# Performance work log

Measured on AMD Instinct MI355X. Metric: run time of the kernel, lower is better.

## Reference

```python
import jax, jax.numpy as jnp
import numpy as np

N, E = 100000, 1600000
IN, HID, OUT = 128, 64, 64
BN_EPS = 1e-5


def setup_inputs() -> dict:
    key = jax.random.key(0)
    ks = jax.random.split(key, 6)
    x = jax.random.normal(ks[0], (N, IN), dtype=jnp.float32)
    edge_index = jax.random.randint(ks[1], (2, E), 0, N, dtype=jnp.int32)
    W1 = jax.random.normal(ks[2], (IN, HID), dtype=jnp.float32) / np.sqrt(IN).astype(np.float32)
    b1 = jnp.zeros((HID,), jnp.float32)
    bn_weight = jnp.ones((HID,), jnp.float32)
    bn_bias = jnp.zeros((HID,), jnp.float32)
    W2 = jax.random.normal(ks[3], (HID, OUT), dtype=jnp.float32) / np.sqrt(HID).astype(np.float32)
    b2 = jnp.zeros((OUT,), jnp.float32)
    return {"x": x, "edge_index": edge_index, "W1": W1, "b1": b1,
            "bn_weight": bn_weight, "bn_bias": bn_bias, "W2": W2, "b2": b2}


def _gcn_conv(x, W, b, src, dst, deg_inv_sqrt):
    # PyG GCNConv: linear first, then symmetric-normalized aggregation with self-loops.
    h = x @ W                                        # [N, out]
    norm = deg_inv_sqrt[src] * deg_inv_sqrt[dst]     # [E]
    agg = jax.ops.segment_sum(h[src] * norm[:, None], dst, num_segments=h.shape[0])
    # self-loop contribution: norm = 1/deg
    agg = agg + h * (deg_inv_sqrt * deg_inv_sqrt)[:, None]
    return agg + b


def reference(x, edge_index, W1, b1, bn_weight, bn_bias, W2, b2):
    src, dst = edge_index[0], edge_index[1]
    # degree including self-loop (GCNConv add_self_loops=True, edge_weight=1)
    deg = jax.ops.segment_sum(jnp.ones((E,), x.dtype), dst, num_segments=N) + 1.0
    deg_inv_sqrt = jax.lax.rsqrt(deg)
    h = _gcn_conv(x, W1, b1, src, dst, deg_inv_sqrt)
    # BatchNorm1d (training-mode batch statistics, biased variance)
    mean = jnp.mean(h, axis=0)
    var = jnp.var(h, axis=0)
    h = (h - mean) * jax.lax.rsqrt(var + BN_EPS) * bn_weight + bn_bias
    h = jax.nn.relu(h)
    # dropout: inference mode (identity)
    return _gcn_conv(h, W2, b2, src, dst, deg_inv_sqrt)
```

## Files before the change

### kernel.cpp

```cpp
#include <hip/hip_runtime.h>

#define N_NODES 100000
#define E_EDGES 1600000
#define IN_F    128
#define HID_F   64
#define OUT_F   64
#define BN_EPS  1e-5f
#define NBUK    391
#define CHUNK   6250
#define NGBLK   3125

__device__ __forceinline__ float bflo(unsigned int u) { return __uint_as_float(u << 16); }
__device__ __forceinline__ float bfhi(unsigned int u) { return __uint_as_float(u & 0xFFFF0000u); }
__device__ __forceinline__ unsigned int pack2bf(float a, float b) {
    unsigned int ua = __float_as_uint(a), ub = __float_as_uint(b);
    ua = (ua + 0x7fffu + ((ua >> 16) & 1u)) >> 16;
    ub = (ub + 0x7fffu + ((ub >> 16) & 1u)) >> 16;
    return ua | (ub << 16);
}
#define ADD8(A, u)                                           \
    do {                                                     \
        A[0] += bflo((u).x); A[1] += bfhi((u).x);            \
        A[2] += bflo((u).y); A[3] += bfhi((u).y);            \
        A[4] += bflo((u).z); A[5] += bfhi((u).z);            \
        A[6] += bflo((u).w); A[7] += bfhi((u).w);            \
    } while (0)

__global__ __launch_bounds__(512) void k_chist(const int* __restrict__ dstv,
                                               int* __restrict__ chist) {
    __shared__ int h[NBUK];
    const int tid = threadIdx.x;
    const int e0 = blockIdx.x * CHUNK;
    for (int b = tid; b < NBUK; b += 512) h[b] = 0;
    __syncthreads();
    for (int t = tid; t < CHUNK; t += 512)
        atomicAdd(&h[dstv[e0 + t] >> 8], 1);
    __syncthreads();
    for (int b = tid; b < NBUK; b += 512)
        if (h[b]) atomicAdd(&chist[b], h[b]);
}

__global__ __launch_bounds__(512) void k_cscan(int* __restrict__ coff,
                                               int* __restrict__ ccur) {
    __shared__ int sh[512];
    const int tid = threadIdx.x;
    int v = (tid < NBUK) ? coff[tid] : 0;
    sh[tid] = v;
    __syncthreads();
    for (int off = 1; off < 512; off <<= 1) {
        int t = (tid >= off) ? sh[tid - off] : 0;
        __syncthreads();
        sh[tid] += t;
        __syncthreads();
    }
    int excl = sh[tid] - v;
    if (tid < NBUK) { coff[tid] = excl; ccur[tid] = excl; }
    if (tid == 0) coff[NBUK] = E_EDGES;
}

__global__ __launch_bounds__(512) void k_bucket(const int* __restrict__ srcv,
                                                const int* __restrict__ dstv,
                                                int* __restrict__ ccur,
                                                unsigned int* __restrict__ aux) {
    __shared__ int dl[CHUNK];
    __shared__ int hist[NBUK], base[NBUK], lcur[NBUK];
    const int tid = threadIdx.x;
    const int e0 = blockIdx.x * CHUNK;
    for (int b = tid; b < NBUK; b += 512) hist[b] = 0;
    __syncthreads();
    for (int t = tid; t < CHUNK; t += 512) {
        int d = dstv[e0 + t];
        dl[t] = d;
        atomicAdd(&hist[d >> 8], 1);
    }
    __syncthreads();
    for (int b = tid; b < NBUK; b += 512) {
        int h = hist[b];
        if (h) base[b] = atomicAdd(&ccur[b], h);
        lcur[b] = 0;
    }
    __syncthreads();
    for (int t = tid; t < CHUNK; t += 512) {
        int d = dl[t];
        int b = d >> 8;
        int off = atomicAdd(&lcur[b], 1);
        aux[base[b] + off] = ((unsigned int)srcv[e0 + t] << 8) | (unsigned int)(d & 255);
    }
}

__global__ __launch_bounds__(256) void k_csrnode(const int* __restrict__ coff,
                                                 const unsigned int* __restrict__ aux,
                                                 int* __restrict__ rowptr,
                                                 float* __restrict__ dis,
                                                 int* __restrict__ csr_src) {
    __shared__ int c0[256], sc[256], cur[256];
    const int tid = threadIdx.x;
    const int n0 = blockIdx.x * 256;
    const int nn = min(256, N_NODES - n0);
    const int estart = coff[blockIdx.x];
    const int eend   = coff[blockIdx.x + 1];
    c0[tid] = 0;
    __syncthreads();
    for (int e = estart + tid; e < eend; e += 256)
        atomicAdd(&c0[aux[e] & 255], 1);
    __syncthreads();
    int v = c0[tid];
    sc[tid] = v;
    __syncthreads();
    for (int off = 1; off < 256; off <<= 1) {
        int t = (tid >= off) ? sc[tid - off] : 0;
        __syncthreads();
        sc[tid] += t;
        __syncthreads();
    }
    int excl = sc[tid] - v;
    if (tid < nn) {
        int p = estart + excl;
        rowptr[n0 + tid] = p;
        cur[tid] = p;
        dis[n0 + tid] = rsqrtf((float)v + 1.0f);
    }
    if (blockIdx.x == NBUK - 1 && tid == 0) rowptr[N_NODES] = E_EDGES;
    __syncthreads();
    for (int e = estart + tid; e < eend; e += 256) {
        unsigned int u = aux[e];
        int pos = atomicAdd(&cur[u & 255], 1);
        csr_src[pos] = (int)(u >> 8);
    }
}

__global__ __launch_bounds__(256) void k_gemm1(const float* __restrict__ x,
                                               const float* __restrict__ W1,
                                               const float* __restrict__ dis,
                                               unsigned short* __restrict__ hs1) {
    __shared__ float Ws[IN_F][HID_F];
    __shared__ float As[64][68];
    const int tid = threadIdx.x;
    const int r0 = blockIdx.x * 64;

#pragma unroll
    for (int p = 0; p < 8; ++p) {
        int idx = p * 256 + tid;
        ((float4*)&Ws[0][0])[idx] = ((const float4*)W1)[idx];
    }

    const int tx = tid & 15, ty = tid >> 4;
    float acc[4][4] = {};

    for (int kk = 0; kk < IN_F; kk += 64) {
        __syncthreads();
#pragma unroll
        for (int p = 0; p < 4; ++p) {
            int idx = p * 256 + tid;
            int row = idx >> 4;
            int c4  = idx & 15;
            float4 v = make_float4(0.f, 0.f, 0.f, 0.f);
            if (r0 + row < N_NODES)
                v = ((const float4*)(x + (size_t)(r0 + row) * IN_F + kk))[c4];
            *(float4*)&As[row][c4 * 4] = v;
        }
        __syncthreads();
#pragma unroll 4
        for (int k2 = 0; k2 < 64; ++k2) {
            int k = kk + k2;
            float4 b = *(const float4*)&Ws[k][tx * 4];
            float a0 = As[ty * 4 + 0][k2];
            float a1 = As[ty * 4 + 1][k2];
            float a2 = As[ty * 4 + 2][k2];
            float a3 = As[ty * 4 + 3][k2];
            acc[0][0] = fmaf(a0, b.x, acc[0][0]); acc[0][1] = fmaf(a0, b.y, acc[0][1]);
            acc[0][2] = fmaf(a0, b.z, acc[0][2]); acc[0][3] = fmaf(a0, b.w, acc[0][3]);
            acc[1][0] = fmaf(a1, b.x, acc[1][0]); acc[1][1] = fmaf(a1, b.y, acc[1][1]);
            acc[1][2] = fmaf(a1, b.z, acc[1][2]); acc[1][3] = fmaf(a1, b.w, acc[1][3]);
            acc[2][0] = fmaf(a2, b.x, acc[2][0]); acc[2][1] = fmaf(a2, b.y, acc[2][1]);
            acc[2][2] = fmaf(a2, b.z, acc[2][2]); acc[2][3] = fmaf(a2, b.w, acc[2][3]);
            acc[3][0] = fmaf(a3, b.x, acc[3][0]); acc[3][1] = fmaf(a3, b.y, acc[3][1]);
            acc[3][2] = fmaf(a3, b.z, acc[3][2]); acc[3][3] = fmaf(a3, b.w, acc[3][3]);
        }
    }
#pragma unroll
    for (int j = 0; j < 4; ++j) {
        int row = r0 + ty * 4 + j;
        if (row < N_NODES) {
            float d = dis[row];
            uint2 o;
            o.x = pack2bf(acc[j][0] * d, acc[j][1] * d);
            o.y = pack2bf(acc[j][2] * d, acc[j][3] * d);
            *(uint2*)&hs1[(size_t)row * HID_F + tx * 4] = o;
        }
    }
}

__global__ __launch_bounds__(256) void k_gather1(const int* __restrict__ rowptr,
                                                 const int* __restrict__ csr_src,
                                                 const unsigned short* __restrict__ hsb,
                                                 const float* __restrict__ dis,
                                                 const float* __restrict__ b1,
                                                 float* __restrict__ agg,
                                                 float* __restrict__ partials) {
    const int tid = threadIdx.x;
    const int g = tid >> 3, q = tid & 7;
    const int n = blockIdx.x * 32 + g;
    const uint4* __restrict__ hs16 = (const uint4*)hsb;

    const int start = rowptr[n], end = rowptr[n + 1];
    float A0[8] = {}, A1[8] = {}, A2[8] = {}, A3[8] = {};
    {
        uint4 u = hs16[(size_t)n * 8 + q];
        ADD8(A0, u);
    }
    int i = start;
    for (; i + 3 < end; i += 4) {
        int s0 = csr_src[i + 0], s1 = csr_src[i + 1];
        int s2 = csr_src[i + 2], s3 = csr_src[i + 3];
        uint4 u0 = hs16[(size_t)s0 * 8 + q];
        uint4 u1 = hs16[(size_t)s1 * 8 + q];
        uint4 u2 = hs16[(size_t)s2 * 8 + q];
        uint4 u3 = hs16[(size_t)s3 * 8 + q];
        ADD8(A0, u0); ADD8(A1, u1); ADD8(A2, u2); ADD8(A3, u3);
    }
    for (; i < end; ++i) {
        uint4 u = hs16[(size_t)csr_src[i] * 8 + q];
        ADD8(A0, u);
    }
    const float d = dis[n];
    const float4 blo = ((const float4*)b1)[q * 2];
    const float4 bhi = ((const float4*)b1)[q * 2 + 1];
    float o[8];
    o[0] = fmaf(d, A0[0] + A1[0] + A2[0] + A3[0], blo.x);
    o[1] = fmaf(d, A0[1] + A1[1] + A2[1] + A3[1], blo.y);
    o[2] = fmaf(d, A0[2] + A1[2] + A2[2] + A3[2], blo.z);
    o[3] = fmaf(d, A0[3] + A1[3] + A2[3] + A3[3], blo.w);
    o[4] = fmaf(d, A0[4] + A1[4] + A2[4] + A3[4], bhi.x);
    o[5] = fmaf(d, A0[5] + A1[5] + A2[5] + A3[5], bhi.y);
    o[6] = fmaf(d, A0[6] + A1[6] + A2[6] + A3[6], bhi.z);
    o[7] = fmaf(d, A0[7] + A1[7] + A2[7] + A3[7], bhi.w);
    float4* ag = (float4*)(agg + (size_t)n * HID_F + q * 8);
    ag[0] = make_float4(o[0], o[1], o[2], o[3]);
    ag[1] = make_float4(o[4], o[5], o[6], o[7]);

    __shared__ float4 redA[256], redB[256];
    redA[tid] = make_float4(o[0], o[1], o[2], o[3]);
    redB[tid] = make_float4(o[4], o[5], o[6], o[7]);
    __syncthreads();
    for (int s = 128; s >= 8; s >>= 1) {
        if (tid < s) {
            redA[tid].x += redA[tid + s].x; redA[tid].y += redA[tid + s].y;
            redA[tid].z += redA[tid + s].z; redA[tid].w += redA[tid + s].w;
            redB[tid].x += redB[tid + s].x; redB[tid].y += redB[tid + s].y;
            redB[tid].z += redB[tid + s].z; redB[tid].w += redB[tid + s].w;
        }
        __syncthreads();
    }
    float4* pr = (float4*)(partials + (size_t)blockIdx.x * 128);
    if (tid < 8) { pr[tid * 2] = redA[tid]; pr[tid * 2 + 1] = redB[tid]; }
    __syncthreads();
    redA[tid] = make_float4(o[0] * o[0], o[1] * o[1], o[2] * o[2], o[3] * o[3]);
    redB[tid] = make_float4(o[4] * o[4], o[5] * o[5], o[6] * o[6], o[7] * o[7]);
    __syncthreads();
    for (int s = 128; s >= 8; s >>= 1) {
        if (tid < s) {
            redA[tid].x += redA[tid + s].x; redA[tid].y += redA[tid + s].y;
            redA[tid].z += redA[tid + s].z; redA[tid].w += redA[tid + s].w;
            redB[tid].x += redB[tid + s].x; redB[tid].y += redB[tid + s].y;
            redB[tid].z += redB[tid + s].z; redB[tid].w += redB[tid + s].w;
        }
        __syncthreads();
    }
    if (tid < 8) { pr[16 + tid * 2] = redA[tid]; pr[16 + tid * 2 + 1] = redB[tid]; }
}

__global__ __launch_bounds__(256) void k_bnfinal(const float* __restrict__ partials,
                                                 float* __restrict__ bnstats) {
    const int tid = threadIdx.x;
    const int col = tid & 127;
    const int half = tid >> 7;
    float s = 0.f;
    for (int r = blockIdx.x * 2 + half; r < NGBLK; r += 128)
        s += partials[(size_t)r * 128 + col];
    __shared__ float sh[256];
    sh[tid] = s;
    __syncthreads();
    if (tid < 128) unsafeAtomicAdd(&bnstats[col], sh[tid] + sh[tid + 128]);
}

__global__ __launch_bounds__(256) void k_gemm2(const float* __restrict__ agg1,
                                               const float* __restrict__ W2,
                                               const float* __restrict__ dis,
                                               const float* __restrict__ bnw,
                                               const float* __restrict__ bnb,
                                               const float* __restrict__ bnstats,
                                               unsigned short* __restrict__ hs2) {
    __shared__ float Ws[HID_F][OUT_F];
    __shared__ float As[64][68];
    __shared__ float scale_s[64], shift_s[64];
    const int tid = threadIdx.x;
    const int r0 = blockIdx.x * 64;

    if (tid < 64) {
        const float invN = 1.0f / (float)N_NODES;
        float mean = bnstats[tid] * invN;
        float var  = bnstats[64 + tid] * invN - mean * mean;
        float sc   = bnw[tid] * rsqrtf(var + BN_EPS);
        scale_s[tid] = sc;
        shift_s[tid] = fmaf(-mean, sc, bnb[tid]);
    }
#pragma unroll
    for (int p = 0; p < 4; ++p) {
        int idx = p * 256 + tid;
        ((float4*)&Ws[0][0])[idx] = ((const float4*)W2)[idx];
    }
    __syncthreads();
#pragma unroll
    for (int p = 0; p < 4; ++p) {
        int idx = p * 256 + tid;
        int row = idx >> 4;
        int c4  = idx & 15;
        float4 v = make_float4(0.f, 0.f, 0.f, 0.f);
        if (r0 + row < N_NODES) {
            v = ((const float4*)(agg1 + (size_t)(r0 + row) * HID_F))[c4];
            int k0 = c4 * 4;
            v.x = fmaxf(fmaf(v.x, scale_s[k0 + 0], shift_s[k0 + 0]), 0.f);
            v.y = fmaxf(fmaf(v.y, scale_s[k0 + 1], shift_s[k0 + 1]), 0.f);
            v.z = fmaxf(fmaf(v.z, scale_s[k0 + 2], shift_s[k0 + 2]), 0.f);
            v.w = fmaxf(fmaf(v.w, scale_s[k0 + 3], shift_s[k0 + 3]), 0.f);
        }
        *(float4*)&As[row][c4 * 4] = v;
    }
    __syncthreads();
    const int tx = tid & 15, ty = tid >> 4;
    float acc[4][4] = {};
#pragma unroll 4
    for (int k = 0; k < HID_F; ++k) {
        float4 b = *(const float4*)&Ws[k][tx * 4];
        float a0 = As[ty * 4 + 0][k];
        float a1 = As[ty * 4 + 1][k];
        float a2 = As[ty * 4 + 2][k];
        float a3 = As[ty * 4 + 3][k];
        acc[0][0] = fmaf(a0, b.x, acc[0][0]); acc[0][1] = fmaf(a0, b.y, acc[0][1]);
        acc[0][2] = fmaf(a0, b.z, acc[0][2]); acc[0][3] = fmaf(a0, b.w, acc[0][3]);
        acc[1][0] = fmaf(a1, b.x, acc[1][0]); acc[1][1] = fmaf(a1, b.y, acc[1][1]);
        acc[1][2] = fmaf(a1, b.z, acc[1][2]); acc[1][3] = fmaf(a1, b.w, acc[1][3]);
        acc[2][0] = fmaf(a2, b.x, acc[2][0]); acc[2][1] = fmaf(a2, b.y, acc[2][1]);
        acc[2][2] = fmaf(a2, b.z, acc[2][2]); acc[2][3] = fmaf(a2, b.w, acc[2][3]);
        acc[3][0] = fmaf(a3, b.x, acc[3][0]); acc[3][1] = fmaf(a3, b.y, acc[3][1]);
        acc[3][2] = fmaf(a3, b.z, acc[3][2]); acc[3][3] = fmaf(a3, b.w, acc[3][3]);
    }
#pragma unroll
    for (int j = 0; j < 4; ++j) {
        int row = r0 + ty * 4 + j;
        if (row < N_NODES) {
            float d = dis[row];
            uint2 o;
            o.x = pack2bf(acc[j][0] * d, acc[j][1] * d);
            o.y = pack2bf(acc[j][2] * d, acc[j][3] * d);
            *(uint2*)&hs2[(size_t)row * OUT_F + tx * 4] = o;
        }
    }
}

__global__ __launch_bounds__(256) void k_gather2(const int* __restrict__ rowptr,
                                                 const int* __restrict__ csr_src,
                                                 const unsigned short* __restrict__ hsb,
                                                 const float* __restrict__ dis,
                                                 const float* __restrict__ b2,
                                                 float* __restrict__ out) {
    const int tid = threadIdx.x;
    const int g = tid >> 3, q = tid & 7;
    const int n = blockIdx.x * 32 + g;
    const uint4* __restrict__ hs16 = (const uint4*)hsb;

    const int start = rowptr[n], end = rowptr[n + 1];
    float A0[8] = {}, A1[8] = {}, A2[8] = {}, A3[8] = {};
    {
        uint4 u = hs16[(size_t)n * 8 + q];
        ADD8(A0, u);
    }
    int i = start;
    for (; i + 3 < end; i += 4) {
        int s0 = csr_src[i + 0], s1 = csr_src[i + 1];
        int s2 = csr_src[i + 2], s3 = csr_src[i + 3];
        uint4 u0 = hs16[(size_t)s0 * 8 + q];
        uint4 u1 = hs16[(size_t)s1 * 8 + q];
        uint4 u2 = hs16[(size_t)s2 * 8 + q];
        uint4 u3 = hs16[(size_t)s3 * 8 + q];
        ADD8(A0, u0); ADD8(A1, u1); ADD8(A2, u2); ADD8(A3, u3);
    }
    for (; i < end; ++i) {
        uint4 u = hs16[(size_t)csr_src[i] * 8 + q];
        ADD8(A0, u);
    }
    const float d = dis[n];
    const float4 blo = ((const float4*)b2)[q * 2];
    const float4 bhi = ((const float4*)b2)[q * 2 + 1];
    float4 o0, o1;
    o0.x = fmaf(d, A0[0] + A1[0] + A2[0] + A3[0], blo.x);
    o0.y = fmaf(d, A0[1] + A1[1] + A2[1] + A3[1], blo.y);
    o0.z = fmaf(d, A0[2] + A1[2] + A2[2] + A3[2], blo.z);
    o0.w = fmaf(d, A0[3] + A1[3] + A2[3] + A3[3], blo.w);
    o1.x = fmaf(d, A0[4] + A1[4] + A2[4] + A3[4], bhi.x);
    o1.y = fmaf(d, A0[5] + A1[5] + A2[5] + A3[5], bhi.y);
    o1.z = fmaf(d, A0[6] + A1[6] + A2[6] + A3[6], bhi.z);
    o1.w = fmaf(d, A0[7] + A1[7] + A2[7] + A3[7], bhi.w);
    float4* op = (float4*)(out + (size_t)n * OUT_F + q * 8);
    op[0] = o0;
    op[1] = o1;
}

extern "C" void kernel_launch(void* const* d_in, const int* in_sizes, int n_in,
                              void* d_out, int out_size, void* d_ws, size_t ws_size,
                              hipStream_t stream) {
    const float* x   = (const float*)d_in[0];
    const int*   ei  = (const int*)d_in[1];
    const float* W1  = (const float*)d_in[2];
    const float* b1  = (const float*)d_in[3];
    const float* bnw = (const float*)d_in[4];
    const float* bnb = (const float*)d_in[5];
    const float* W2  = (const float*)d_in[6];
    const float* b2  = (const float*)d_in[7];
    float* out = (float*)d_out;

    float* ws = (float*)d_ws;
    float*        dis     = ws;
    int*          rowptr  = (int*)(ws + 100352);
    int*          coff    = (int*)(ws + 100352 + 100608);
    int*          ccur    = (int*)(ws + 100352 + 100608 + 512);
    float*        bnstats = ws + 100352 + 100608 + 512 + 512;
    int*          csr_src = (int*)(ws + 100352 + 100608 + 512 + 512 + 128);
    float*        bufA    = ws + 100352 + 100608 + 512 + 512 + 128 + 1600000;
    float*        bufB    = bufA + (size_t)N_NODES * HID_F;
    unsigned int*  aux  = (unsigned int*)bufA;
    unsigned short* hsb = (unsigned short*)bufA;
    float* partials = out;

    const int* srcv = ei;
    const int* dstv = ei + E_EDGES;

    hipMemsetAsync(coff, 0, (NBUK + 1) * sizeof(int), stream);
    hipMemsetAsync(bnstats, 0, 128 * sizeof(float), stream);

    k_chist  <<<256, 512, 0, stream>>>(dstv, coff);
    k_cscan  <<<1, 512, 0, stream>>>(coff, ccur);
    k_bucket <<<256, 512, 0, stream>>>(srcv, dstv, ccur, aux);
    k_csrnode<<<NBUK, 256, 0, stream>>>(coff, aux, rowptr, dis, csr_src);

    k_gemm1  <<<(N_NODES + 63) / 64, 256, 0, stream>>>(x, W1, dis, hsb);
    k_gather1<<<NGBLK, 256, 0, stream>>>(rowptr, csr_src, hsb, dis, b1, bufB, partials);
    k_bnfinal<<<64, 256, 0, stream>>>(partials, bnstats);
    k_gemm2  <<<(N_NODES + 63) / 64, 256, 0, stream>>>(bufB, W2, dis, bnw, bnb, bnstats, hsb);
    k_gather2<<<NGBLK, 256, 0, stream>>>(rowptr, csr_src, hsb, dis, b2, out);
}
```

Measured before the change: 275.7 us.

## Use bf16 MFMA for both node-feature GEMMs with LDS-staged coalesced output

Replaces the scalar FP32 FMA tiles in both dense GEMM kernels with bf16 MFMA 16x16x32 instructions. Inputs and weights are converted to bf16 in shared memory, and results are staged through LDS so global stores are 16-byte coalesced. The intent is to cut compute and LDS traffic in the GEMM stages. In exchange, the GEMM inputs lose precision to bf16, and each block transposes the weights with scalar stores.

```diff
diff --git a/kernel.cpp b/kernel.cpp
--- a/kernel.cpp
+++ b/kernel.cpp
@@ -9,6 +9,10 @@
 #define NBUK    391
 #define CHUNK   6250
 #define NGBLK   3125
+#define NMBLK   1563
+
+typedef __bf16 bf16x8 __attribute__((ext_vector_type(8)));
+typedef float  f32x4  __attribute__((ext_vector_type(4)));
 
 __device__ __forceinline__ float bflo(unsigned int u) { return __uint_as_float(u << 16); }
 __device__ __forceinline__ float bfhi(unsigned int u) { return __uint_as_float(u & 0xFFFF0000u); }
@@ -18,6 +22,10 @@
     ub = (ub + 0x7fffu + ((ub >> 16) & 1u)) >> 16;
     return ua | (ub << 16);
 }
+__device__ __forceinline__ unsigned short bf1(float a) {
+    unsigned int ua = __float_as_uint(a);
+    return (unsigned short)((ua + 0x7fffu + ((ua >> 16) & 1u)) >> 16);
+}
 #define ADD8(A, u)                                           \
     do {                                                     \
         A[0] += bflo((u).x); A[1] += bfhi((u).x);            \
@@ -133,61 +141,64 @@
                                                const float* __restrict__ W1,
                                                const float* __restrict__ dis,
                                                unsigned short* __restrict__ hs1) {
-    __shared__ float Ws[IN_F][HID_F];
-    __shared__ float As[64][68];
+    __shared__ unsigned short Asb[64 * 136];
+    __shared__ unsigned short Btb[64 * 136];
+    __shared__ unsigned short Cc[64 * 72];
+    __shared__ float disS[64];
     const int tid = threadIdx.x;
     const int r0 = blockIdx.x * 64;
 
-#pragma unroll
-    for (int p = 0; p < 8; ++p) {
+    if (tid < 64) disS[tid] = (r0 + tid < N_NODES) ? dis[r0 + tid] : 0.f;
+
+    const float4* x4 = (const float4*)x;
+#pragma unroll
+    for (int p = 0; p < 4; ++p) {
+        int idx8 = p * 256 + tid;
+        int row = idx8 >> 4, c8 = idx8 & 15;
+        float4 v0 = make_float4(0.f, 0.f, 0.f, 0.f), v1 = v0;
+        if (r0 + row < N_NODES) {
+            v0 = x4[(size_t)(r0 + row) * 32 + c8 * 2];
+            v1 = x4[(size_t)(r0 + row) * 32 + c8 * 2 + 1];
+        }
+        uint4 u;
+        u.x = pack2bf(v0.x, v0.y); u.y = pack2bf(v0.z, v0.w);
+        u.z = pack2bf(v1.x, v1.y); u.w = pack2bf(v1.z, v1.w);
+        *(uint4*)&Asb[row * 136 + c8 * 8] = u;
+    }
+    for (int idx = tid; idx < IN_F * HID_F; idx += 256) {
+        int k = idx >> 6, n = idx & 63;
+        Btb[n * 136 + k] = bf1(W1[idx]);
+    }
+    __syncthreads();
+
+    const int wv = tid >> 6, lane = tid & 63;
+    const int m = lane & 15, quad = lane >> 4;
+    const int arow = wv * 16 + m;
+    f32x4 acc[4] = {};
+#pragma unroll
+    for (int ks = 0; ks < 4; ++ks) {
+        int k0 = ks * 32 + quad * 8;
+        bf16x8 af = *(const bf16x8*)&Asb[arow * 136 + k0];
+#pragma unroll
+        for (int c = 0; c < 4; ++c) {
+            bf16x8 bfr = *(const bf16x8*)&Btb[(c * 16 + m) * 136 + k0];
+            acc[c] = __builtin_amdgcn_mfma_f32_16x16x32_bf16(af, bfr, acc[c], 0, 0, 0);
+        }
+    }
+#pragma unroll
+    for (int c = 0; c < 4; ++c)
+#pragma unroll
+        for (int r = 0; r < 4; ++r) {
+            int rl = wv * 16 + quad * 4 + r;
+            Cc[rl * 72 + c * 16 + m] = bf1(acc[c][r] * disS[rl]);
+        }
+    __syncthreads();
+#pragma unroll
+    for (int p = 0; p < 2; ++p) {
         int idx = p * 256 + tid;
-        ((float4*)&Ws[0][0])[idx] = ((const float4*)W1)[idx];
-    }
-
-    const int tx = tid & 15, ty = tid >> 4;
-    float acc[4][4] = {};
-
-    for (int kk = 0; kk < IN_F; kk += 64) {
-        __syncthreads();
-#pragma unroll
-        for (int p = 0; p < 4; ++p) {
-            int idx = p * 256 + tid;
-            int row = idx >> 4;
-            int c4  = idx & 15;
-            float4 v = make_float4(0.f, 0.f, 0.f, 0.f);
-            if (r0 + row < N_NODES)
-                v = ((const float4*)(x + (size_t)(r0 + row) * IN_F + kk))[c4];
-            *(float4*)&As[row][c4 * 4] = v;
-        }
-        __syncthreads();
-#pragma unroll 4
-        for (int k2 = 0; k2 < 64; ++k2) {
-            int k = kk + k2;
-            float4 b = *(const float4*)&Ws[k][tx * 4];
-            float a0 = As[ty * 4 + 0][k2];
-            float a1 = As[ty * 4 + 1][k2];
-            float a2 = As[ty * 4 + 2][k2];
-            float a3 = As[ty * 4 + 3][k2];
-            acc[0][0] = fmaf(a0, b.x, acc[0][0]); acc[0][1] = fmaf(a0, b.y, acc[0][1]);
-            acc[0][2] = fmaf(a0, b.z, acc[0][2]); acc[0][3] = fmaf(a0, b.w, acc[0][3]);
-            acc[1][0] = fmaf(a1, b.x, acc[1][0]); acc[1][1] = fmaf(a1, b.y, acc[1][1]);
-            acc[1][2] = fmaf(a1, b.z, acc[1][2]); acc[1][3] = fmaf(a1, b.w, acc[1][3]);
-            acc[2][0] = fmaf(a2, b.x, acc[2][0]); acc[2][1] = fmaf(a2, b.y, acc[2][1]);
-            acc[2][2] = fmaf(a2, b.z, acc[2][2]); acc[2][3] = fmaf(a2, b.w, acc[2][3]);
-            acc[3][0] = fmaf(a3, b.x, acc[3][0]); acc[3][1] = fmaf(a3, b.y, acc[3][1]);
-            acc[3][2] = fmaf(a3, b.z, acc[3][2]); acc[3][3] = fmaf(a3, b.w, acc[3][3]);
-        }
-    }
-#pragma unroll
-    for (int j = 0; j < 4; ++j) {
-        int row = r0 + ty * 4 + j;
-        if (row < N_NODES) {
-            float d = dis[row];
-            uint2 o;
-            o.x = pack2bf(acc[j][0] * d, acc[j][1] * d);
-            o.y = pack2bf(acc[j][2] * d, acc[j][3] * d);
-            *(uint2*)&hs1[(size_t)row * HID_F + tx * 4] = o;
-        }
+        int row = idx >> 3, c8 = idx & 7;
+        if (r0 + row < N_NODES)
+            *(uint4*)&hs1[(size_t)(r0 + row) * 64 + c8 * 8] = *(uint4*)&Cc[row * 72 + c8 * 8];
     }
 }
 
@@ -291,9 +302,10 @@
                                                const float* __restrict__ bnb,
                                                const float* __restrict__ bnstats,
                                                unsigned short* __restrict__ hs2) {
-    __shared__ float Ws[HID_F][OUT_F];
-    __shared__ float As[64][68];
-    __shared__ float scale_s[64], shift_s[64];
+    __shared__ unsigned short Ab[64 * 72];
+    __shared__ unsigned short Bt2[64 * 72];
+    __shared__ unsigned short Cc[64 * 72];
+    __shared__ float scale_s[64], shift_s[64], disS[64];
     const int tid = threadIdx.x;
     const int r0 = blockIdx.x * 64;
 
@@ -304,58 +316,60 @@
         float sc   = bnw[tid] * rsqrtf(var + BN_EPS);
         scale_s[tid] = sc;
         shift_s[tid] = fmaf(-mean, sc, bnb[tid]);
-    }
+        disS[tid] = (r0 + tid < N_NODES) ? dis[r0 + tid] : 0.f;
+    }
+    for (int idx = tid; idx < HID_F * OUT_F; idx += 256) {
+        int k = idx >> 6, n = idx & 63;
+        Bt2[n * 72 + k] = bf1(W2[idx]);
+    }
+    __syncthreads();
+
+    const float4* a4 = (const float4*)agg1;
 #pragma unroll
     for (int p = 0; p < 4; ++p) {
+        int idx4 = p * 256 + tid;
+        int row = idx4 >> 4, c4 = idx4 & 15;
+        float4 v = make_float4(0.f, 0.f, 0.f, 0.f);
+        if (r0 + row < N_NODES) v = a4[(size_t)(r0 + row) * 16 + c4];
+        int k0 = c4 * 4;
+        v.x = fmaxf(fmaf(v.x, scale_s[k0 + 0], shift_s[k0 + 0]), 0.f);
+        v.y = fmaxf(fmaf(v.y, scale_s[k0 + 1], shift_s[k0 + 1]), 0.f);
+        v.z = fmaxf(fmaf(v.z, scale_s[k0 + 2], shift_s[k0 + 2]), 0.f);
+        v.w = fmaxf(fmaf(v.w, scale_s[k0 + 3], shift_s[k0 + 3]), 0.f);
+        uint2 u;
+        u.x = pack2bf(v.x, v.y); u.y = pack2bf(v.z, v.w);
+        *(uint2*)&Ab[row * 72 + c4 * 4] = u;
+    }
+    __syncthreads();
+
+    const int wv = tid >> 6, lane = tid & 63;
+    const int m = lane & 15, quad = lane >> 4;
+    const int arow = wv * 16 + m;
+    f32x4 acc[4] = {};
+#pragma unroll
+    for (int ks = 0; ks < 2; ++ks) {
+        int k0 = ks * 32 + quad * 8;
+        bf16x8 af = *(const bf16x8*)&Ab[arow * 72 + k0];
+#pragma unroll
+        for (int c = 0; c < 4; ++c) {
+            bf16x8 bfr = *(const bf16x8*)&Bt2[(c * 16 + m) * 72 + k0];
+            acc[c] = __builtin_amdgcn_mfma_f32_16x16x32_bf16(af, bfr, acc[c], 0, 0, 0);
+        }
+    }
+#pragma unroll
+    for (int c = 0; c < 4; ++c)
+#pragma unroll
+        for (int r = 0; r < 4; ++r) {
+            int rl = wv * 16 + quad * 4 + r;
+            Cc[rl * 72 + c * 16 + m] = bf1(acc[c][r] * disS[rl]);
+        }
+    __syncthreads();
+#pragma unroll
+    for (int p = 0; p < 2; ++p) {
         int idx = p * 256 + tid;
-        ((float4*)&Ws[0][0])[idx] = ((const float4*)W2)[idx];
-    }
-    __syncthreads();
-#pragma unroll
-    for (int p = 0; p < 4; ++p) {
-        int idx = p * 256 + tid;
-        int row = idx >> 4;
-        int c4  = idx & 15;
-        float4 v = make_float4(0.f, 0.f, 0.f, 0.f);
-        if (r0 + row < N_NODES) {
-            v = ((const float4*)(agg1 + (size_t)(r0 + row) * HID_F))[c4];
-            int k0 = c4 * 4;
-            v.x = fmaxf(fmaf(v.x, scale_s[k0 + 0], shift_s[k0 + 0]), 0.f);
-            v.y = fmaxf(fmaf(v.y, scale_s[k0 + 1], shift_s[k0 + 1]), 0.f);
-            v.z = fmaxf(fmaf(v.z, scale_s[k0 + 2], shift_s[k0 + 2]), 0.f);
-            v.w = fmaxf(fmaf(v.w, scale_s[k0 + 3], shift_s[k0 + 3]), 0.f);
-        }
-        *(float4*)&As[row][c4 * 4] = v;
-    }
-    __syncthreads();
-    const int tx = tid & 15, ty = tid >> 4;
-    float acc[4][4] = {};
-#pragma unroll 4
-    for (int k = 0; k < HID_F; ++k) {
-        float4 b = *(const float4*)&Ws[k][tx * 4];
-        float a0 = As[ty * 4 + 0][k];
-        float a1 = As[ty * 4 + 1][k];
-        float a2 = As[ty * 4 + 2][k];
-        float a3 = As[ty * 4 + 3][k];
-        acc[0][0] = fmaf(a0, b.x, acc[0][0]); acc[0][1] = fmaf(a0, b.y, acc[0][1]);
-        acc[0][2] = fmaf(a0, b.z, acc[0][2]); acc[0][3] = fmaf(a0, b.w, acc[0][3]);
-        acc[1][0] = fmaf(a1, b.x, acc[1][0]); acc[1][1] = fmaf(a1, b.y, acc[1][1]);
-        acc[1][2] = fmaf(a1, b.z, acc[1][2]); acc[1][3] = fmaf(a1, b.w, acc[1][3]);
-        acc[2][0] = fmaf(a2, b.x, acc[2][0]); acc[2][1] = fmaf(a2, b.y, acc[2][1]);
-        acc[2][2] = fmaf(a2, b.z, acc[2][2]); acc[2][3] = fmaf(a2, b.w, acc[2][3]);
-        acc[3][0] = fmaf(a3, b.x, acc[3][0]); acc[3][1] = fmaf(a3, b.y, acc[3][1]);
-        acc[3][2] = fmaf(a3, b.z, acc[3][2]); acc[3][3] = fmaf(a3, b.w, acc[3][3]);
-    }
-#pragma unroll
-    for (int j = 0; j < 4; ++j) {
-        int row = r0 + ty * 4 + j;
-        if (row < N_NODES) {
-            float d = dis[row];
-            uint2 o;
-            o.x = pack2bf(acc[j][0] * d, acc[j][1] * d);
-            o.y = pack2bf(acc[j][2] * d, acc[j][3] * d);
-            *(uint2*)&hs2[(size_t)row * OUT_F + tx * 4] = o;
-        }
+        int row = idx >> 3, c8 = idx & 7;
+        if (r0 + row < N_NODES)
+            *(uint4*)&hs2[(size_t)(r0 + row) * 64 + c8 * 8] = *(uint4*)&Cc[row * 72 + c8 * 8];
     }
 }
 
@@ -444,9 +458,9 @@
     k_bucket <<<256, 512, 0, stream>>>(srcv, dstv, ccur, aux);
     k_csrnode<<<NBUK, 256, 0, stream>>>(coff, aux, rowptr, dis, csr_src);
 
-    k_gemm1  <<<(N_NODES + 63) / 64, 256, 0, stream>>>(x, W1, dis, hsb);
+    k_gemm1  <<<NMBLK, 256, 0, stream>>>(x, W1, dis, hsb);
     k_gather1<<<NGBLK, 256, 0, stream>>>(rowptr, csr_src, hsb, dis, b1, bufB, partials);
     k_bnfinal<<<64, 256, 0, stream>>>(partials, bnstats);
-    k_gemm2  <<<(N_NODES + 63) / 64, 256, 0, stream>>>(bufB, W2, dis, bnw, bnb, bnstats, hsb);
+    k_gemm2  <<<NMBLK, 256, 0, stream>>>(bufB, W2, dis, bnw, bnb, bnstats, hsb);
     k_gather2<<<NGBLK, 256, 0, stream>>>(rowptr, csr_src, hsb, dis, b2, out);
 }
```

Result: faster. 254.6 us (-7.7%).
